# Performance work log

Hardware: AMD Instinct MI355X
Metric: run time of the kernel (lower is better)

The kernel has to match this reference:

```python
import jax, jax.numpy as jnp
import numpy as np

KSIZE = 11
SIGMA = 1.5
PAD = KSIZE // 2
C1 = 0.01 ** 2
C2 = 0.03 ** 2


def gaussian_kernel(ksize, sigma):
    ax = np.arange(ksize, dtype=np.float32) - (ksize - 1) / 2.0
    g = np.exp(-(ax ** 2) / (2.0 * sigma ** 2))
    k2d = np.outer(g, g)
    k2d = k2d / k2d.sum()
    # depthwise kernel for 3 channels: [out=3, in/groups=1, kh, kw]
    return jnp.asarray(np.broadcast_to(k2d, (3, 1, ksize, ksize)).copy())


def dwconv(x, kernel):
    # x: [B,3,H,W], kernel: [3,1,k,k], 'same' padding, groups=3
    return jax.lax.conv_general_dilated(
        x, kernel,
        window_strides=(1, 1),
        padding=[(PAD, PAD), (PAD, PAD)],
        dimension_numbers=('NCHW', 'OIHW', 'NCHW'),
        feature_group_count=3)


def setup_inputs() -> dict:
    key = jax.random.key(0)
    k1, k2 = jax.random.split(key)
    shape = (16, 3, 512, 512)
    img_output = jax.random.uniform(k1, shape, dtype=jnp.float32)
    img_target = jax.random.uniform(k2, shape, dtype=jnp.float32)
    kernel = gaussian_kernel(KSIZE, SIGMA)
    return {"img_output": img_output, "img_target": img_target, "kernel": kernel}


def reference(img_output, img_target, kernel):
    s, t = img_output, img_target
    ux = dwconv(s, kernel)
    uy = dwconv(t, kernel)
    uxx = dwconv(s * s, kernel)
    uyy = dwconv(t * t, kernel)
    uxy = dwconv(s * t, kernel)
    ssim = ((2 * ux * uy + C1) * (2 * (uxy - ux * uy) + C2)
            / (ux ** 2 + uy ** 2 + C1)
            / (uxx - ux * ux + (uyy - uy * uy) + C2))
    return 1.0 - ssim.mean()
```

## Files before the change

kernel.cpp:

```cpp
#include <hip/hip_runtime.h>
#include <stdint.h>

typedef _Float16 f16;
typedef f16  f16x8 __attribute__((ext_vector_type(8)));
typedef f16  f16x4 __attribute__((ext_vector_type(4)));
typedef f16  f16x2 __attribute__((ext_vector_type(2)));
typedef float f32x4 __attribute__((ext_vector_type(4)));

#define W 512
#define H 512
#define KS 11
#define NW 8
#define NBLK 256
#define NITER 12
#define NLINES 256
#define C1_SSIM 0.0001f
#define C2_SSIM 0.0009f
#define NTOTAL 12582912.0f

#define LCOLS 80

__device__ __constant__ const float GW[KS] = {
    1.02838e-3f, 7.59876e-3f, 3.600076e-2f, 1.0936069e-1f, 2.1300554e-1f,
    2.6601172e-1f,
    2.1300554e-1f, 1.0936069e-1f, 3.600076e-2f, 7.59876e-3f, 1.02838e-3f
};

__device__ inline float ssim_px(float ux, float uy, float uxx, float uyy, float uxy) {
    const float uxuy = ux * uy;
    const float a = 2.f * uxuy + C1_SSIM;
    const float b = 2.f * (uxy - uxuy) + C2_SSIM;
    const float c = ux * ux + uy * uy + C1_SSIM;
    const float d = (uxx - ux * ux) + (uyy - uy * uy) + C2_SSIM;
    return (a * b) * __builtin_amdgcn_rcpf(c * d);
}

__device__ __forceinline__ f16x8 pack84(f32x4 a, f32x4 b) {
    f16x8 r;
    f16x2 h;
    h = __builtin_bit_cast(f16x2, __builtin_amdgcn_cvt_pkrtz(a[0], a[1]));
    r[0] = h[0]; r[1] = h[1];
    h = __builtin_bit_cast(f16x2, __builtin_amdgcn_cvt_pkrtz(a[2], a[3]));
    r[2] = h[0]; r[3] = h[1];
    h = __builtin_bit_cast(f16x2, __builtin_amdgcn_cvt_pkrtz(b[0], b[1]));
    r[4] = h[0]; r[5] = h[1];
    h = __builtin_bit_cast(f16x2, __builtin_amdgcn_cvt_pkrtz(b[2], b[3]));
    r[6] = h[0]; r[7] = h[1];
    return r;
}

__device__ __forceinline__ void issue_dma(const float* __restrict__ simg,
                                          const float* __restrict__ timg,
                                          const float* __restrict__ zb,
                                          int w, int lane, int T, float* ldsbase) {
    const int z  = T >> 6;
    const int rr = T & 63;
    const int ty = rr >> 3;
    const int tx = rr & 7;
    const float* sp = simg + ((size_t)z << 18);
    const float* tp = timg + ((size_t)z << 18);
    const int ybase = (ty << 6) - 5;
    const int xbase = (tx << 6) - 8;
    #pragma unroll
    for (int k = 0; k < 7; ++k) {
        const int c = (k << 3) + w;
        if (c < 50) {
            const int img = (c >= 25) ? 1 : 0;
            const int cc  = img ? (c - 25) : c;
            const int off = (cc << 10) + (lane << 4);
            const int t16 = off >> 6;
            const int row = (t16 * 205) >> 10;
            const int colb = off - row * 320;
            const int ry   = ybase + row;
            const int gcol = xbase + (colb >> 2);
            const float* src = img ? tp : sp;
            const bool ok = ((unsigned)ry < (unsigned)H) &
                            ((unsigned)gcol <= (unsigned)(W - 4));
            const float* ga = ok ? (src + ((size_t)ry << 9) + gcol) : zb;
            void* ldst = (char*)ldsbase + (c << 10);
            __builtin_amdgcn_global_load_lds(
                (const uint32_t __attribute__((address_space(1)))*)ga,
                (uint32_t __attribute__((address_space(3)))*)ldst,
                16, 0, 0);
        }
    }
}

__device__ __forceinline__ float compute_half(const float* __restrict__ base,
                                              int coff, int n, int h,
                                              f16x8 af, f16x4 a1v, f16x4 a2v) {
    union H4 { f16x4 v4; f16x2 v2[2]; };
    const float* ls = base + coff;
    const float* lt = base + 6400 + coff;
    f16x4 ph[2][5];
    float sum = 0.f;
    #pragma unroll
    for (int j = 0; j < 3; ++j) {
        const int g  = (h << 1) + j;
        const int ro = ((g << 4) + n) * LCOLS;
        const f32x4 s0 = *(const f32x4*)(ls + ro);
        const f32x4 s1 = *(const f32x4*)(ls + ro + 4);
        const f32x4 t0 = *(const f32x4*)(lt + ro);
        const f32x4 t1 = *(const f32x4*)(lt + ro + 4);
        const f16x8 sf = pack84(s0, s1);
        const f16x8 tf = pack84(t0, t1);
        const int pb = j & 1;
        #pragma unroll
        for (int c = 0; c < 5; ++c) {
            f16x8 ch;
            if      (c == 0) ch = sf;
            else if (c == 1) ch = tf;
            else if (c == 2) ch = sf * sf;
            else if (c == 3) ch = tf * tf;
            else             ch = sf * tf;
            const f32x4 zero = {0.f, 0.f, 0.f, 0.f};
            const f32x4 d = __builtin_amdgcn_mfma_f32_16x16x32_f16(ch, af, zero, 0, 0, 0);
            H4 u;
            u.v2[0] = __builtin_bit_cast(f16x2, __builtin_amdgcn_cvt_pkrtz(d[0], d[1]));
            u.v2[1] = __builtin_bit_cast(f16x2, __builtin_amdgcn_cvt_pkrtz(d[2], d[3]));
            ph[pb][c] = u.v4;
        }
        if (j >= 1) {
            const int pa = pb ^ 1;
            f32x4 acc[5];
            #pragma unroll
            for (int c = 0; c < 5; ++c) {
                const f32x4 zero = {0.f, 0.f, 0.f, 0.f};
                f32x4 a = __builtin_amdgcn_mfma_f32_16x16x16f16(a2v, ph[pb][c], zero, 0, 0, 0);
                a = __builtin_amdgcn_mfma_f32_16x16x16f16(a1v, ph[pa][c], a, 0, 0, 0);
                acc[c] = a;
            }
            #pragma unroll
            for (int rg = 0; rg < 4; ++rg)
                sum += ssim_px(acc[0][rg], acc[1][rg], acc[2][rg],
                               acc[3][rg], acc[4][rg]);
        }
    }
    return sum;
}

__global__ __launch_bounds__(512, 1)
void ssim_main(const float* __restrict__ simg, const float* __restrict__ timg,
               float* __restrict__ accum, const float* __restrict__ zbuf) {
    __shared__ __align__(16) float lds[2][2 * 6400];
    __shared__ float red[NW];

    const int tid  = threadIdx.x;
    const int w    = tid >> 6;
    const int lane = tid & 63;
    const int n    = lane & 15;
    const int q    = lane >> 4;
    const int h    = w >> 2;
    const int cw   = w & 3;
    const int bid  = blockIdx.x;

    issue_dma(simg, timg, zbuf, w, lane, bid, &lds[0][0]);
    __builtin_amdgcn_sched_barrier(0);

    f16x8 af;
    #pragma unroll
    for (int j = 0; j < 8; ++j) {
        const int k = (q << 3) + j;
        const int d = k - n - 3;
        af[j] = (d >= 0 && d < KS) ? (f16)GW[d] : (f16)0.f;
    }
    f16x4 a1v, a2v;
    #pragma unroll
    for (int j = 0; j < 4; ++j) {
        const int k  = (q << 2) + j;
        const int d1 = k - n;
        const int d2 = k + 16 - n;
        a1v[j] = (d1 >= 0 && d1 < KS) ? (f16)GW[d1] : (f16)0.f;
        a2v[j] = (d2 >= 0 && d2 < KS) ? (f16)GW[d2] : (f16)0.f;
    }

    const int coff = (cw << 4) + (q << 3);
    float sum = 0.f;

    for (int t = 0; t < NITER; ++t) {
        if (t < NITER - 1) {
            issue_dma(simg, timg, zbuf, w, lane, bid + ((t + 1) << 8),
                      &lds[(t + 1) & 1][0]);
            __builtin_amdgcn_sched_barrier(0);
            asm volatile("s_waitcnt vmcnt(6)" ::: "memory");
        } else {
            asm volatile("s_waitcnt vmcnt(0)" ::: "memory");
        }
        __builtin_amdgcn_s_barrier();
        __builtin_amdgcn_sched_barrier(0);

        sum += compute_half(&lds[t & 1][0], coff, n, h, af, a1v, a2v);

        __builtin_amdgcn_sched_barrier(0);
        __builtin_amdgcn_s_barrier();
    }

    #pragma unroll
    for (int off = 32; off > 0; off >>= 1)
        sum += __shfl_down(sum, off, 64);
    if (lane == 0) red[w] = sum;
    __syncthreads();
    if (tid == 0) {
        float bs = 0.f;
        #pragma unroll
        for (int i = 0; i < NW; ++i) bs += red[i];
        accum[bid << 4] = bs;
    }
}

__global__ void ssim_final(const float* __restrict__ accum, float* __restrict__ out) {
    const int lane = threadIdx.x;
    float s = 0.f;
    #pragma unroll
    for (int i = 0; i < NLINES / 64; ++i)
        s += accum[((i << 6) + lane) << 4];
    #pragma unroll
    for (int off = 32; off > 0; off >>= 1)
        s += __shfl_down(s, off, 64);
    if (lane == 0) out[0] = 1.f - s * (1.f / NTOTAL);
}

extern "C" void kernel_launch(void* const* d_in, const int* in_sizes, int n_in,
                              void* d_out, int out_size, void* d_ws, size_t ws_size,
                              hipStream_t stream) {
    const float* s = (const float*)d_in[0];
    const float* t = (const float*)d_in[1];
    float* out   = (float*)d_out;
    float* accum = (float*)d_ws;
    const float* zbuf = accum + NLINES * 16;

    hipMemsetAsync(accum, 0, NLINES * 16 * sizeof(float) + 256, stream);
    ssim_main<<<dim3(NBLK), 512, 0, stream>>>(s, t, accum, zbuf);
    ssim_final<<<1, 64, 0, stream>>>(accum, out);
}
```

Measured before the change: 137.5 us.

## Halve tile height, double block count, and remap blocks for higher occupancy

Tiles shrink from 64 to 32 output rows, so the launch uses 512 blocks and each block stages less LDS per buffer (two images of 48 rows by 80 columns). Launch bounds now request 4 blocks per CU instead of 1, with a block index remap to spread neighbouring tiles across blocks. Partial sums from blocks sharing a slot are merged with atomicAdd. The aim is more resident waves to hide load latency. The cost is a larger vertical halo overhead per tile (48 rows loaded for 32 output rows) and some atomic contention.

After: 130.9 us. 4.8% less time.

```diff
diff --git a/kernel.cpp b/kernel.cpp
--- a/kernel.cpp
+++ b/kernel.cpp
@@ -11,7 +11,7 @@
 #define H 512
 #define KS 11
 #define NW 8
-#define NBLK 256
+#define NBLK 512
 #define NITER 12
 #define NLINES 256
 #define C1_SSIM 0.0001f
@@ -19,6 +19,9 @@
 #define NTOTAL 12582912.0f
 
 #define LCOLS 80
+#define IMGF32 3840
+#define TILEF32 7680
+#define NCHUNK 30
 
 __device__ __constant__ const float GW[KS] = {
     1.02838e-3f, 7.59876e-3f, 3.600076e-2f, 1.0936069e-1f, 2.1300554e-1f,
@@ -53,20 +56,20 @@
                                           const float* __restrict__ timg,
                                           const float* __restrict__ zb,
                                           int w, int lane, int T, float* ldsbase) {
-    const int z  = T >> 6;
-    const int rr = T & 63;
+    const int z  = T >> 7;
+    const int rr = T & 127;
     const int ty = rr >> 3;
     const int tx = rr & 7;
     const float* sp = simg + ((size_t)z << 18);
     const float* tp = timg + ((size_t)z << 18);
-    const int ybase = (ty << 6) - 5;
+    const int ybase = (ty << 5) - 5;
     const int xbase = (tx << 6) - 8;
     #pragma unroll
-    for (int k = 0; k < 7; ++k) {
+    for (int k = 0; k < 4; ++k) {
         const int c = (k << 3) + w;
-        if (c < 50) {
-            const int img = (c >= 25) ? 1 : 0;
-            const int cc  = img ? (c - 25) : c;
+        if (c < NCHUNK) {
+            const int img = (c >= 15) ? 1 : 0;
+            const int cc  = img ? (c - 15) : c;
             const int off = (cc << 10) + (lane << 4);
             const int t16 = off >> 6;
             const int row = (t16 * 205) >> 10;
@@ -77,7 +80,7 @@
             const bool ok = ((unsigned)ry < (unsigned)H) &
                             ((unsigned)gcol <= (unsigned)(W - 4));
             const float* ga = ok ? (src + ((size_t)ry << 9) + gcol) : zb;
-            void* ldst = (char*)ldsbase + (c << 10);
+            void* ldst = (char*)ldsbase + img * (IMGF32 * 4) + (cc << 10);
             __builtin_amdgcn_global_load_lds(
                 (const uint32_t __attribute__((address_space(1)))*)ga,
                 (uint32_t __attribute__((address_space(3)))*)ldst,
@@ -86,25 +89,22 @@
     }
 }
 
-__device__ __forceinline__ float compute_half(const float* __restrict__ base,
+__device__ __forceinline__ float compute_part(const float* __restrict__ base,
                                               int coff, int n, int h,
                                               f16x8 af, f16x4 a1v, f16x4 a2v) {
     union H4 { f16x4 v4; f16x2 v2[2]; };
     const float* ls = base + coff;
-    const float* lt = base + 6400 + coff;
+    const float* lt = base + IMGF32 + coff;
     f16x4 ph[2][5];
-    float sum = 0.f;
-    #pragma unroll
-    for (int j = 0; j < 3; ++j) {
-        const int g  = (h << 1) + j;
-        const int ro = ((g << 4) + n) * LCOLS;
+    #pragma unroll
+    for (int j = 0; j < 2; ++j) {
+        const int ro = (((h + j) << 4) + n) * LCOLS;
         const f32x4 s0 = *(const f32x4*)(ls + ro);
         const f32x4 s1 = *(const f32x4*)(ls + ro + 4);
         const f32x4 t0 = *(const f32x4*)(lt + ro);
         const f32x4 t1 = *(const f32x4*)(lt + ro + 4);
         const f16x8 sf = pack84(s0, s1);
         const f16x8 tf = pack84(t0, t1);
-        const int pb = j & 1;
         #pragma unroll
         for (int c = 0; c < 5; ++c) {
             f16x8 ch;
@@ -118,31 +118,29 @@
             H4 u;
             u.v2[0] = __builtin_bit_cast(f16x2, __builtin_amdgcn_cvt_pkrtz(d[0], d[1]));
             u.v2[1] = __builtin_bit_cast(f16x2, __builtin_amdgcn_cvt_pkrtz(d[2], d[3]));
-            ph[pb][c] = u.v4;
+            ph[j][c] = u.v4;
         }
-        if (j >= 1) {
-            const int pa = pb ^ 1;
-            f32x4 acc[5];
-            #pragma unroll
-            for (int c = 0; c < 5; ++c) {
-                const f32x4 zero = {0.f, 0.f, 0.f, 0.f};
-                f32x4 a = __builtin_amdgcn_mfma_f32_16x16x16f16(a2v, ph[pb][c], zero, 0, 0, 0);
-                a = __builtin_amdgcn_mfma_f32_16x16x16f16(a1v, ph[pa][c], a, 0, 0, 0);
-                acc[c] = a;
-            }
-            #pragma unroll
-            for (int rg = 0; rg < 4; ++rg)
-                sum += ssim_px(acc[0][rg], acc[1][rg], acc[2][rg],
-                               acc[3][rg], acc[4][rg]);
-        }
-    }
+    }
+    float sum = 0.f;
+    f32x4 acc[5];
+    #pragma unroll
+    for (int c = 0; c < 5; ++c) {
+        const f32x4 zero = {0.f, 0.f, 0.f, 0.f};
+        f32x4 a = __builtin_amdgcn_mfma_f32_16x16x16f16(a2v, ph[1][c], zero, 0, 0, 0);
+        a = __builtin_amdgcn_mfma_f32_16x16x16f16(a1v, ph[0][c], a, 0, 0, 0);
+        acc[c] = a;
+    }
+    #pragma unroll
+    for (int rg = 0; rg < 4; ++rg)
+        sum += ssim_px(acc[0][rg], acc[1][rg], acc[2][rg],
+                       acc[3][rg], acc[4][rg]);
     return sum;
 }
 
-__global__ __launch_bounds__(512, 1)
+__global__ __launch_bounds__(512, 4)
 void ssim_main(const float* __restrict__ simg, const float* __restrict__ timg,
                float* __restrict__ accum, const float* __restrict__ zbuf) {
-    __shared__ __align__(16) float lds[2][2 * 6400];
+    __shared__ __align__(16) float lds[2][TILEF32];
     __shared__ float red[NW];
 
     const int tid  = threadIdx.x;
@@ -152,9 +150,11 @@
     const int q    = lane >> 4;
     const int h    = w >> 2;
     const int cw   = w & 3;
-    const int bid  = blockIdx.x;
-
-    issue_dma(simg, timg, zbuf, w, lane, bid, &lds[0][0]);
+
+    const int bid = blockIdx.x;
+    const int L   = (bid & 7) * (NBLK / 8) + (bid >> 3);
+
+    issue_dma(simg, timg, zbuf, w, lane, L, &lds[0][0]);
     __builtin_amdgcn_sched_barrier(0);
 
     f16x8 af;
@@ -179,17 +179,17 @@
 
     for (int t = 0; t < NITER; ++t) {
         if (t < NITER - 1) {
-            issue_dma(simg, timg, zbuf, w, lane, bid + ((t + 1) << 8),
+            issue_dma(simg, timg, zbuf, w, lane, L + ((t + 1) << 9),
                       &lds[(t + 1) & 1][0]);
             __builtin_amdgcn_sched_barrier(0);
-            asm volatile("s_waitcnt vmcnt(6)" ::: "memory");
+            asm volatile("s_waitcnt vmcnt(3)" ::: "memory");
         } else {
             asm volatile("s_waitcnt vmcnt(0)" ::: "memory");
         }
         __builtin_amdgcn_s_barrier();
         __builtin_amdgcn_sched_barrier(0);
 
-        sum += compute_half(&lds[t & 1][0], coff, n, h, af, a1v, a2v);
+        sum += compute_part(&lds[t & 1][0], coff, n, h, af, a1v, a2v);
 
         __builtin_amdgcn_sched_barrier(0);
         __builtin_amdgcn_s_barrier();
@@ -204,7 +204,7 @@
         float bs = 0.f;
         #pragma unroll
         for (int i = 0; i < NW; ++i) bs += red[i];
-        accum[bid << 4] = bs;
+        atomicAdd(&accum[(bid & (NLINES - 1)) << 4], bs);
     }
 }
 
```
